# Performance work log

Measured on AMD Instinct MI355X. Metric: run time of the kernel, lower is better.

The kernel has to match this reference:

```python
import jax, jax.numpy as jnp
import numpy as np

B, T, I, H, L, O = 8192, 204, 5, 24, 10, 612

def setup_inputs() -> dict:
    key = jax.random.key(0)
    ks = jax.random.split(key, 10)
    s_ih = 1.0 / np.sqrt(H)
    inp = {
        "x": jax.random.normal(ks[0], (B, T, I), dtype=jnp.float32),
        # torch nn.LSTM params: weight_ih_l0 [4H,I], weight_hh_l0 [4H,H], biases [4H]
        "W_ih": jax.random.uniform(ks[1], (4 * H, I), jnp.float32, -s_ih, s_ih),
        "W_hh": jax.random.uniform(ks[2], (4 * H, H), jnp.float32, -s_ih, s_ih),
        "b_ih": jax.random.uniform(ks[3], (4 * H,), jnp.float32, -s_ih, s_ih),
        "b_hh": jax.random.uniform(ks[4], (4 * H,), jnp.float32, -s_ih, s_ih),
        "fc0_w": jax.random.uniform(ks[5], (L, H * T), jnp.float32, -1 / np.sqrt(H * T), 1 / np.sqrt(H * T)),
        "fc0_b": jax.random.uniform(ks[6], (L,), jnp.float32, -1 / np.sqrt(H * T), 1 / np.sqrt(H * T)),
        "out_w": jax.random.uniform(ks[7], (O, L), jnp.float32, -1 / np.sqrt(L), 1 / np.sqrt(L)),
        "out_b": jax.random.uniform(ks[8], (O,), jnp.float32, -1 / np.sqrt(L), 1 / np.sqrt(L)),
    }
    return inp

def _lstm_forward(x, W_ih, W_hh, b_ih, b_hh):
    # Precompute input projections for all timesteps: [B,T,4H] -> time-major [T,B,4H]
    x_proj = jnp.einsum("bti,gi->btg", x, W_ih) + b_ih
    x_proj = jnp.swapaxes(x_proj, 0, 1)
    h0 = jnp.zeros((x.shape[0], W_hh.shape[1]), x.dtype)
    c0 = jnp.zeros_like(h0)

    def step(carry, xt):
        h, c = carry
        gates = xt + h @ W_hh.T + b_hh  # [B,4H]; torch gate order i,f,g,o
        i, f, g, o = jnp.split(gates, 4, axis=-1)
        c = jax.nn.sigmoid(f) * c + jax.nn.sigmoid(i) * jnp.tanh(g)
        h = jax.nn.sigmoid(o) * jnp.tanh(c)
        return (h, c), h

    _, hs = jax.lax.scan(step, (h0, c0), x_proj)  # hs: [T,B,H]
    return jnp.swapaxes(hs, 0, 1)  # [B,T,H]

def reference(x, W_ih, W_hh, b_ih, b_hh, fc0_w, fc0_b, out_w, out_b):
    h = _lstm_forward(x, W_ih, W_hh, b_ih, b_hh)       # [B,T,H]
    h = h.reshape(h.shape[0], -1)                       # [B, T*H]
    h = jax.nn.relu(h @ fc0_w.T + fc0_b)                # [B, L]
    return h @ out_w.T + out_b                          # [B, O]
```

## Files before the change

kernel.cpp:

```cpp
#include <hip/hip_runtime.h>
#include <math.h>

#define T_  204
#define I_  5
#define H_  24
#define L_  10
#define O_  612
#define Bsz 8192

typedef _Float16 half8 __attribute__((ext_vector_type(8)));
typedef _Float16 half2t __attribute__((ext_vector_type(2)));
typedef float    float4t __attribute__((ext_vector_type(4)));

union U16B { float4t f4; half8 h8; float f[4]; _Float16 h[8]; half2t h2[4]; };

__device__ __forceinline__ float fast_rcp(float x){ return __builtin_amdgcn_rcpf(x); }
__device__ __forceinline__ float fast_ex2(float x){ return __builtin_amdgcn_exp2f(x); }
__device__ __forceinline__ half2t pk2(float a, float b){
    return __builtin_bit_cast(half2t, __builtin_amdgcn_cvt_pkrtz(a, b));
}

#define MFMA16(a,b,c) __builtin_amdgcn_mfma_f32_16x16x32_f16((a),(b),(c),0,0,0)

#define L2E  1.44269504f
#define L2E2 2.88539008f

__device__ __forceinline__ float sigm2(float x){ return fast_rcp(1.f + fast_ex2(x * -L2E)); }
__device__ __forceinline__ float tanh2(float x){ return 2.f * fast_rcp(1.f + fast_ex2(x * -L2E2)) - 1.f; }

__device__ __forceinline__ int unit_of(int q, int T) {
    return (q < 3) ? (8*q + T) : (8*(T >> 1) + 6 + (T & 1));
}

__global__ __launch_bounds__(64)
void pack_fc0(const float* __restrict__ fc0_w, float4t* __restrict__ dst)
{
    const int t = blockIdx.x, lane = threadIdx.x;
    const int m = lane & 15, q = lane >> 4;
    U16B v;
    #pragma unroll
    for (int i = 0; i < 8; ++i) {
        const int k = 8*q + i;
        float f = (m < L_ && k < H_) ? fc0_w[m*(T_*H_) + t*H_ + k] : 0.0f;
        v.h[i] = (_Float16)f;
    }
    dst[t*64 + lane] = v.f4;
}

__global__ __launch_bounds__(64)
void lstm_mfma(const float* __restrict__ x,
               const float* __restrict__ W_ih,
               const float* __restrict__ W_hh,
               const float* __restrict__ b_ih,
               const float* __restrict__ b_hh,
               const float* __restrict__ fc0_b,
               const float* __restrict__ out_w,
               const float* __restrict__ out_b,
               const float4t* __restrict__ fc0A,
               float* __restrict__ out)
{
    __shared__ __align__(16) _Float16 actL[16*24];

    const int lane = threadIdx.x;
    const int m = lane & 15;
    const int q = lane >> 4;
    const int elem = blockIdx.x * 16 + m;

    const float4t zf4 = {0.f, 0.f, 0.f, 0.f};

    half8 Ag[6];
    #pragma unroll
    for (int T6 = 0; T6 < 6; ++T6) {
        const int u = unit_of(m >> 2, T6);
        const int srow = (m & 3) * H_ + u;
        float wv[8];
        if (q < 3) {
            const float4t* pw = (const float4t*)(W_hh + srow*H_ + 8*q);
            float4t wa = pw[0], wb = pw[1];
            #pragma unroll
            for (int i = 0; i < 4; ++i) { wv[i] = wa[i]; wv[4+i] = wb[i]; }
        } else {
            #pragma unroll
            for (int i = 0; i < 8; ++i) wv[i] = 0.f;
            #pragma unroll
            for (int i = 0; i < I_; ++i) wv[i] = W_ih[srow*I_ + i];
            wv[5] = b_ih[srow] + b_hh[srow];
        }
        U16B tw;
        #pragma unroll
        for (int i = 0; i < 8; ++i) tw.h[i] = (_Float16)wv[i];
        Ag[T6] = tw.h8;
    }

    const float* xp = x + (size_t)elem * (T_*I_);

    U16B B;
    if (q == 3) {
        B.h2[0] = pk2(xp[0], xp[1]);
        B.h2[1] = pk2(xp[2], xp[3]);
        B.h2[2] = pk2(xp[4], 1.0f);
        B.h2[3] = pk2(0.f, 0.f);
    } else {
        B.f4 = zf4;
    }
    float xC[I_] = {0,0,0,0,0};
    if (q == 3) {
        #pragma unroll
        for (int i = 0; i < I_; ++i) xC[i] = xp[I_ + i];
    }

    float c_[6] = {0,0,0,0,0,0};
    float4t accF = zf4;
    float4t fa = fc0A[lane];

    for (int t = 0; t < T_; ++t) {
        const int tn = (t + 1 < T_) ? t + 1 : t;
        const float4t fan = fc0A[tn*64 + lane];
        float xN[I_] = {0,0,0,0,0};
        if (q == 3) {
            const int tp2 = (t + 2 < T_) ? t + 2 : T_ - 1;
            const float* xq = xp + tp2*I_;
            #pragma unroll
            for (int i = 0; i < I_; ++i) xN[i] = xq[i];
        }

        float4t D0 = MFMA16(Ag[0], B.h8, zf4);
        float4t D1 = MFMA16(Ag[1], B.h8, zf4);
        float4t D2 = MFMA16(Ag[2], B.h8, zf4);
        float4t D3 = MFMA16(Ag[3], B.h8, zf4);
        float4t D4 = MFMA16(Ag[4], B.h8, zf4);
        float4t D5 = MFMA16(Ag[5], B.h8, zf4);

        float hh[6];
        {
            float4t D[6] = {D0, D1, D2, D3, D4, D5};
            #pragma unroll
            for (int T6 = 0; T6 < 6; ++T6) {
                const float si = sigm2(D[T6][0]);
                const float sf = sigm2(D[T6][1]);
                const float tg = tanh2(D[T6][2]);
                const float so = sigm2(D[T6][3]);
                c_[T6] = fmaf(sf, c_[T6], si * tg);
                hh[T6] = so * tanh2(c_[T6]);
            }
        }

        const float P0 = __builtin_bit_cast(float, pk2(hh[0], hh[1]));
        const float P1 = __builtin_bit_cast(float, pk2(hh[2], hh[3]));
        const float P2 = __builtin_bit_cast(float, pk2(hh[4], hh[5]));

        const int src = 48 + m;
        const float r0 = __shfl(P0, src, 64);
        const float r1 = __shfl(P1, src, 64);
        const float r2 = __shfl(P2, src, 64);
        const float rcv = (q == 0) ? r0 : ((q == 1) ? r1 : r2);

        if (q < 3) {
            B.h2[0] = __builtin_bit_cast(half2t, P0);
            B.h2[1] = __builtin_bit_cast(half2t, P1);
            B.h2[2] = __builtin_bit_cast(half2t, P2);
            B.h2[3] = __builtin_bit_cast(half2t, rcv);
        } else {
            B.h2[0] = pk2(xC[0], xC[1]);
            B.h2[1] = pk2(xC[2], xC[3]);
            B.h2[2] = pk2(xC[4], 1.0f);
            B.h2[3] = pk2(0.f, 0.f);
        }

        U16B fF; fF.f4 = fa;
        accF = MFMA16(fF.h8, B.h8, accF);

        fa = fan;
        #pragma unroll
        for (int i = 0; i < I_; ++i) xC[i] = xN[i];
    }

    float av[4];
    #pragma unroll
    for (int r = 0; r < 4; ++r) {
        const int l = 4*q + r;
        const float fb = (l < L_) ? fc0_b[l] : 0.f;
        const float v = accF[r] + fb;
        av[r] = (l < L_) ? fmaxf(v, 0.f) : 0.f;
    }
    *(half2t*)(&actL[m*24 + 4*q])     = pk2(av[0], av[1]);
    *(half2t*)(&actL[m*24 + 4*q + 2]) = pk2(av[2], av[3]);
    __builtin_amdgcn_wave_barrier();

    U16B Ba;
    if (q < 2) Ba.f4 = *(const float4t*)(&actL[m*24 + q*8]);
    else       Ba.f4 = zf4;

    for (int Tt = 0; Tt < 39; ++Tt) {
        const int row = 16*Tt + m;
        float w0=0.f,w1=0.f,w2=0.f,w3=0.f,w4=0.f,w5=0.f,w6=0.f,w7=0.f;
        if (row < O_ && q < 2) {
            const float2* p2 = (const float2*)(out_w + row*L_);
            if (q == 0) {
                float2 a = p2[0], b = p2[1], cc = p2[2], dd = p2[3];
                w0=a.x; w1=a.y; w2=b.x; w3=b.y; w4=cc.x; w5=cc.y; w6=dd.x; w7=dd.y;
            } else {
                float2 a = p2[4];
                w0=a.x; w1=a.y;
            }
        }
        U16B Aw;
        Aw.h2[0] = pk2(w0,w1); Aw.h2[1] = pk2(w2,w3);
        Aw.h2[2] = pk2(w4,w5); Aw.h2[3] = pk2(w6,w7);

        float4t dd = MFMA16(Aw.h8, Ba.h8, zf4);

        const int ob = 16*Tt + 4*q;
        if (ob < O_) {
            const float4t bias = *(const float4t*)(out_b + ob);
            #pragma unroll
            for (int r = 0; r < 4; ++r) dd[r] += bias[r];
            *(float4t*)(out + (size_t)elem*O_ + ob) = dd;
        }
    }
}

extern "C" void kernel_launch(void* const* d_in, const int* in_sizes, int n_in,
                              void* d_out, int out_size, void* d_ws, size_t ws_size,
                              hipStream_t stream)
{
    const float* x     = (const float*)d_in[0];
    const float* W_ih  = (const float*)d_in[1];
    const float* W_hh  = (const float*)d_in[2];
    const float* b_ih  = (const float*)d_in[3];
    const float* b_hh  = (const float*)d_in[4];
    const float* fc0_w = (const float*)d_in[5];
    const float* fc0_b = (const float*)d_in[6];
    const float* out_w = (const float*)d_in[7];
    const float* out_b = (const float*)d_in[8];
    float* out = (float*)d_out;
    (void)ws_size;

    pack_fc0<<<dim3(T_), dim3(64), 0, stream>>>(fc0_w, (float4t*)d_ws);
    lstm_mfma<<<dim3(Bsz/16), dim3(64), 0, stream>>>(
        x, W_ih, W_hh, b_ih, b_hh, fc0_b, out_w, out_b,
        (const float4t*)d_ws, out);
}
```

Before: 221.9 us.

## Process two batch tiles per wave to interleave independent LSTM recurrences

Each wave now handles 32 batch elements as two independent 16-element tiles, interleaving their MFMAs, gate activations and shuffles to expose instruction-level parallelism in the serial time recurrence. The time loop is unrolled by two with alternating prefetch buffers for x and fc0 weights. The grid is halved, so latency hiding shifts from multiple waves per CU to ILP within one wave, at the cost of higher register use and fewer waves.

After: 357.4 us. 61.1% more time.

```diff
diff --git a/kernel.cpp b/kernel.cpp
--- a/kernel.cpp
+++ b/kernel.cpp
@@ -47,7 +47,89 @@
     dst[t*64 + lane] = v.f4;
 }
 
-__global__ __launch_bounds__(64)
+#define BCH(x) __builtin_bit_cast(half2t, (x))
+
+#define LSTM_STEP(tcur, xCA, xCB, facur)                                        \
+  {                                                                             \
+    float4t DA0 = MFMA16(Ag[0], BA.h8, zf4);                                    \
+    float4t DB0 = MFMA16(Ag[0], BB.h8, zf4);                                    \
+    float4t DA1 = MFMA16(Ag[1], BA.h8, zf4);                                    \
+    float4t DB1 = MFMA16(Ag[1], BB.h8, zf4);                                    \
+    float4t DA2 = MFMA16(Ag[2], BA.h8, zf4);                                    \
+    float4t DB2 = MFMA16(Ag[2], BB.h8, zf4);                                    \
+    float4t DA3 = MFMA16(Ag[3], BA.h8, zf4);                                    \
+    float4t DB3 = MFMA16(Ag[3], BB.h8, zf4);                                    \
+    float4t DA4 = MFMA16(Ag[4], BA.h8, zf4);                                    \
+    float4t DB4 = MFMA16(Ag[4], BB.h8, zf4);                                    \
+    float4t DA5 = MFMA16(Ag[5], BA.h8, zf4);                                    \
+    float4t DB5 = MFMA16(Ag[5], BB.h8, zf4);                                    \
+    float4t DAv[6] = {DA0, DA1, DA2, DA3, DA4, DA5};                            \
+    float4t DBv[6] = {DB0, DB1, DB2, DB3, DB4, DB5};                            \
+    float hA[6];                                                                \
+    float hB[6];                                                                \
+    _Pragma("unroll")                                                           \
+    for (int T6 = 0; T6 < 6; ++T6) {                                            \
+      const float siA = sigm2(DAv[T6][0]);                                      \
+      const float siB = sigm2(DBv[T6][0]);                                      \
+      const float sfA = sigm2(DAv[T6][1]);                                      \
+      const float sfB = sigm2(DBv[T6][1]);                                      \
+      const float tgA = tanh2(DAv[T6][2]);                                      \
+      const float tgB = tanh2(DBv[T6][2]);                                      \
+      const float soA = sigm2(DAv[T6][3]);                                      \
+      const float soB = sigm2(DBv[T6][3]);                                      \
+      cA[T6] = fmaf(sfA, cA[T6], siA * tgA);                                    \
+      cB[T6] = fmaf(sfB, cB[T6], siB * tgB);                                    \
+      hA[T6] = soA * tanh2(cA[T6]);                                             \
+      hB[T6] = soB * tanh2(cB[T6]);                                             \
+    }                                                                           \
+    const float PA0 = __builtin_bit_cast(float, pk2(hA[0], hA[1]));             \
+    const float PA1 = __builtin_bit_cast(float, pk2(hA[2], hA[3]));             \
+    const float PA2 = __builtin_bit_cast(float, pk2(hA[4], hA[5]));             \
+    const float PB0 = __builtin_bit_cast(float, pk2(hB[0], hB[1]));             \
+    const float PB1 = __builtin_bit_cast(float, pk2(hB[2], hB[3]));             \
+    const float PB2 = __builtin_bit_cast(float, pk2(hB[4], hB[5]));             \
+    const int srcl = 48 + m;                                                    \
+    const float rA0 = __shfl(PA0, srcl, 64);                                    \
+    const float rA1 = __shfl(PA1, srcl, 64);                                    \
+    const float rA2 = __shfl(PA2, srcl, 64);                                    \
+    const float rB0 = __shfl(PB0, srcl, 64);                                    \
+    const float rB1 = __shfl(PB1, srcl, 64);                                    \
+    const float rB2 = __shfl(PB2, srcl, 64);                                    \
+    const float rcvA = (q == 0) ? rA0 : ((q == 1) ? rA1 : rA2);                 \
+    const float rcvB = (q == 0) ? rB0 : ((q == 1) ? rB1 : rB2);                 \
+    if (q < 3) {                                                                \
+      BA.h2[0] = BCH(PA0); BA.h2[1] = BCH(PA1);                                 \
+      BA.h2[2] = BCH(PA2); BA.h2[3] = BCH(rcvA);                                \
+      BB.h2[0] = BCH(PB0); BB.h2[1] = BCH(PB1);                                 \
+      BB.h2[2] = BCH(PB2); BB.h2[3] = BCH(rcvB);                                \
+    } else {                                                                    \
+      BA.h2[0] = pk2(xCA[0], xCA[1]);                                           \
+      BA.h2[1] = pk2(xCA[2], xCA[3]);                                           \
+      BA.h2[2] = pk2(xCA[4], 1.0f);                                             \
+      BA.h2[3] = pk2(0.f, 0.f);                                                 \
+      BB.h2[0] = pk2(xCB[0], xCB[1]);                                           \
+      BB.h2[1] = pk2(xCB[2], xCB[3]);                                           \
+      BB.h2[2] = pk2(xCB[4], 1.0f);                                             \
+      BB.h2[3] = pk2(0.f, 0.f);                                                 \
+    }                                                                           \
+    U16B fF; fF.f4 = facur;                                                     \
+    accFA = MFMA16(fF.h8, BA.h8, accFA);                                        \
+    accFB = MFMA16(fF.h8, BB.h8, accFB);                                        \
+    {                                                                           \
+      const int tpx = ((tcur) + 3 < T_) ? (tcur) + 3 : (T_ - 1);                \
+      if (q == 3) {                                                             \
+        _Pragma("unroll")                                                       \
+        for (int i = 0; i < I_; ++i) {                                          \
+          xCA[i] = xpA[tpx * I_ + i];                                           \
+          xCB[i] = xpB[tpx * I_ + i];                                           \
+        }                                                                       \
+      }                                                                         \
+      const int tfx = ((tcur) + 2 < T_) ? (tcur) + 2 : (T_ - 1);                \
+      facur = fc0A[tfx * 64 + lane];                                            \
+    }                                                                           \
+  }
+
+__global__ __launch_bounds__(64, 1)
 void lstm_mfma(const float* __restrict__ x,
                const float* __restrict__ W_ih,
                const float* __restrict__ W_hh,
@@ -59,12 +141,13 @@
                const float4t* __restrict__ fc0A,
                float* __restrict__ out)
 {
-    __shared__ __align__(16) _Float16 actL[16*24];
+    __shared__ __align__(16) _Float16 actL[32*24];
 
     const int lane = threadIdx.x;
     const int m = lane & 15;
     const int q = lane >> 4;
-    const int elem = blockIdx.x * 16 + m;
+    const int elemA = blockIdx.x * 32 + m;
+    const int elemB = elemA + 16;
 
     const float4t zf4 = {0.f, 0.f, 0.f, 0.f};
 
@@ -92,104 +175,71 @@
         Ag[T6] = tw.h8;
     }
 
-    const float* xp = x + (size_t)elem * (T_*I_);
-
-    U16B B;
+    const float* xpA = x + (size_t)elemA * (T_*I_);
+    const float* xpB = x + (size_t)elemB * (T_*I_);
+
+    U16B BA, BB;
     if (q == 3) {
-        B.h2[0] = pk2(xp[0], xp[1]);
-        B.h2[1] = pk2(xp[2], xp[3]);
-        B.h2[2] = pk2(xp[4], 1.0f);
-        B.h2[3] = pk2(0.f, 0.f);
+        BA.h2[0] = pk2(xpA[0], xpA[1]);
+        BA.h2[1] = pk2(xpA[2], xpA[3]);
+        BA.h2[2] = pk2(xpA[4], 1.0f);
+        BA.h2[3] = pk2(0.f, 0.f);
+        BB.h2[0] = pk2(xpB[0], xpB[1]);
+        BB.h2[1] = pk2(xpB[2], xpB[3]);
+        BB.h2[2] = pk2(xpB[4], 1.0f);
+        BB.h2[3] = pk2(0.f, 0.f);
     } else {
-        B.f4 = zf4;
-    }
-    float xC[I_] = {0,0,0,0,0};
+        BA.f4 = zf4;
+        BB.f4 = zf4;
+    }
+
+    float xEA[I_] = {0,0,0,0,0}, xOA[I_] = {0,0,0,0,0};
+    float xEB[I_] = {0,0,0,0,0}, xOB[I_] = {0,0,0,0,0};
     if (q == 3) {
         #pragma unroll
-        for (int i = 0; i < I_; ++i) xC[i] = xp[I_ + i];
-    }
-
-    float c_[6] = {0,0,0,0,0,0};
-    float4t accF = zf4;
-    float4t fa = fc0A[lane];
-
-    for (int t = 0; t < T_; ++t) {
-        const int tn = (t + 1 < T_) ? t + 1 : t;
-        const float4t fan = fc0A[tn*64 + lane];
-        float xN[I_] = {0,0,0,0,0};
-        if (q == 3) {
-            const int tp2 = (t + 2 < T_) ? t + 2 : T_ - 1;
-            const float* xq = xp + tp2*I_;
-            #pragma unroll
-            for (int i = 0; i < I_; ++i) xN[i] = xq[i];
-        }
-
-        float4t D0 = MFMA16(Ag[0], B.h8, zf4);
-        float4t D1 = MFMA16(Ag[1], B.h8, zf4);
-        float4t D2 = MFMA16(Ag[2], B.h8, zf4);
-        float4t D3 = MFMA16(Ag[3], B.h8, zf4);
-        float4t D4 = MFMA16(Ag[4], B.h8, zf4);
-        float4t D5 = MFMA16(Ag[5], B.h8, zf4);
-
-        float hh[6];
-        {
-            float4t D[6] = {D0, D1, D2, D3, D4, D5};
-            #pragma unroll
-            for (int T6 = 0; T6 < 6; ++T6) {
-                const float si = sigm2(D[T6][0]);
-                const float sf = sigm2(D[T6][1]);
-                const float tg = tanh2(D[T6][2]);
-                const float so = sigm2(D[T6][3]);
-                c_[T6] = fmaf(sf, c_[T6], si * tg);
-                hh[T6] = so * tanh2(c_[T6]);
-            }
-        }
-
-        const float P0 = __builtin_bit_cast(float, pk2(hh[0], hh[1]));
-        const float P1 = __builtin_bit_cast(float, pk2(hh[2], hh[3]));
-        const float P2 = __builtin_bit_cast(float, pk2(hh[4], hh[5]));
-
-        const int src = 48 + m;
-        const float r0 = __shfl(P0, src, 64);
-        const float r1 = __shfl(P1, src, 64);
-        const float r2 = __shfl(P2, src, 64);
-        const float rcv = (q == 0) ? r0 : ((q == 1) ? r1 : r2);
-
-        if (q < 3) {
-            B.h2[0] = __builtin_bit_cast(half2t, P0);
-            B.h2[1] = __builtin_bit_cast(half2t, P1);
-            B.h2[2] = __builtin_bit_cast(half2t, P2);
-            B.h2[3] = __builtin_bit_cast(half2t, rcv);
-        } else {
-            B.h2[0] = pk2(xC[0], xC[1]);
-            B.h2[1] = pk2(xC[2], xC[3]);
-            B.h2[2] = pk2(xC[4], 1.0f);
-            B.h2[3] = pk2(0.f, 0.f);
-        }
-
-        U16B fF; fF.f4 = fa;
-        accF = MFMA16(fF.h8, B.h8, accF);
-
-        fa = fan;
-        #pragma unroll
-        for (int i = 0; i < I_; ++i) xC[i] = xN[i];
-    }
-
-    float av[4];
+        for (int i = 0; i < I_; ++i) {
+            xEA[i] = xpA[1*I_ + i];
+            xOA[i] = xpA[2*I_ + i];
+            xEB[i] = xpB[1*I_ + i];
+            xOB[i] = xpB[2*I_ + i];
+        }
+    }
+
+    float cA[6] = {0,0,0,0,0,0};
+    float cB[6] = {0,0,0,0,0,0};
+    float4t accFA = zf4, accFB = zf4;
+    float4t fa0 = fc0A[lane];
+    float4t fa1 = fc0A[64 + lane];
+
+    for (int t = 0; t < T_; t += 2) {
+        LSTM_STEP(t,     xEA, xEB, fa0)
+        LSTM_STEP(t + 1, xOA, xOB, fa1)
+    }
+
+    float avA[4], avB[4];
     #pragma unroll
     for (int r = 0; r < 4; ++r) {
         const int l = 4*q + r;
         const float fb = (l < L_) ? fc0_b[l] : 0.f;
-        const float v = accF[r] + fb;
-        av[r] = (l < L_) ? fmaxf(v, 0.f) : 0.f;
-    }
-    *(half2t*)(&actL[m*24 + 4*q])     = pk2(av[0], av[1]);
-    *(half2t*)(&actL[m*24 + 4*q + 2]) = pk2(av[2], av[3]);
+        const float vA = accFA[r] + fb;
+        const float vB = accFB[r] + fb;
+        avA[r] = (l < L_) ? fmaxf(vA, 0.f) : 0.f;
+        avB[r] = (l < L_) ? fmaxf(vB, 0.f) : 0.f;
+    }
+    *(half2t*)(&actL[m*24 + 4*q])          = pk2(avA[0], avA[1]);
+    *(half2t*)(&actL[m*24 + 4*q + 2])      = pk2(avA[2], avA[3]);
+    *(half2t*)(&actL[(16+m)*24 + 4*q])     = pk2(avB[0], avB[1]);
+    *(half2t*)(&actL[(16+m)*24 + 4*q + 2]) = pk2(avB[2], avB[3]);
     __builtin_amdgcn_wave_barrier();
 
-    U16B Ba;
-    if (q < 2) Ba.f4 = *(const float4t*)(&actL[m*24 + q*8]);
-    else       Ba.f4 = zf4;
+    U16B BaA, BaB;
+    if (q < 2) {
+        BaA.f4 = *(const float4t*)(&actL[m*24 + q*8]);
+        BaB.f4 = *(const float4t*)(&actL[(16+m)*24 + q*8]);
+    } else {
+        BaA.f4 = zf4;
+        BaB.f4 = zf4;
+    }
 
     for (int Tt = 0; Tt < 39; ++Tt) {
         const int row = 16*Tt + m;
@@ -208,14 +258,16 @@
         Aw.h2[0] = pk2(w0,w1); Aw.h2[1] = pk2(w2,w3);
         Aw.h2[2] = pk2(w4,w5); Aw.h2[3] = pk2(w6,w7);
 
-        float4t dd = MFMA16(Aw.h8, Ba.h8, zf4);
+        float4t dA = MFMA16(Aw.h8, BaA.h8, zf4);
+        float4t dB = MFMA16(Aw.h8, BaB.h8, zf4);
 
         const int ob = 16*Tt + 4*q;
         if (ob < O_) {
             const float4t bias = *(const float4t*)(out_b + ob);
             #pragma unroll
-            for (int r = 0; r < 4; ++r) dd[r] += bias[r];
-            *(float4t*)(out + (size_t)elem*O_ + ob) = dd;
+            for (int r = 0; r < 4; ++r) { dA[r] += bias[r]; dB[r] += bias[r]; }
+            *(float4t*)(out + (size_t)elemA*O_ + ob) = dA;
+            *(float4t*)(out + (size_t)elemB*O_ + ob) = dB;
         }
     }
 }
@@ -237,7 +289,7 @@
     (void)ws_size;
 
     pack_fc0<<<dim3(T_), dim3(64), 0, stream>>>(fc0_w, (float4t*)d_ws);
-    lstm_mfma<<<dim3(Bsz/16), dim3(64), 0, stream>>>(
+    lstm_mfma<<<dim3(Bsz/32), dim3(64), 0, stream>>>(
         x, W_ih, W_hh, b_ih, b_hh, fc0_b, out_w, out_b,
         (const float4t*)d_ws, out);
 }
```

## Split LSTM gate tiles across two waves with LDS double-buffered hidden exchange

Applied to the files above, without the earlier changes.

Each 16-element batch tile is now handled by two waves instead of one. Each wave computes three of the six gate MFMA tiles and their activations, and the hidden state is exchanged through a double-buffered LDS buffer with a workgroup barrier every timestep, replacing the cross-lane shuffles. The aim is to halve the serial per-step activation and MFMA work on the recurrence critical path. In exchange it adds an s_barrier and LDS round trip on every step, and the number of resident waves doubles.

After: 218.8 us. No clear change (-1.4%).

```diff
diff --git a/kernel.cpp b/kernel.cpp
--- a/kernel.cpp
+++ b/kernel.cpp
@@ -47,7 +47,54 @@
     dst[t*64 + lane] = v.f4;
 }
 
-__global__ __launch_bounds__(64)
+#define LSTM_STEP(tcur, xC, facur)                                              \
+  {                                                                             \
+    float4t D0 = MFMA16(Ag[0], B.h8, zf4);                                      \
+    float4t D1 = MFMA16(Ag[1], B.h8, zf4);                                      \
+    float4t D2 = MFMA16(Ag[2], B.h8, zf4);                                      \
+    float hh0, hh1, hh2;                                                        \
+    {                                                                           \
+      const float si0 = sigm2(D0[0]), sf0 = sigm2(D0[1]);                       \
+      const float tg0 = tanh2(D0[2]), so0 = sigm2(D0[3]);                       \
+      cc0 = fmaf(sf0, cc0, si0 * tg0);  hh0 = so0 * tanh2(cc0);                 \
+      const float si1 = sigm2(D1[0]), sf1 = sigm2(D1[1]);                       \
+      const float tg1 = tanh2(D1[2]), so1 = sigm2(D1[3]);                       \
+      cc1 = fmaf(sf1, cc1, si1 * tg1);  hh1 = so1 * tanh2(cc1);                 \
+      const float si2 = sigm2(D2[0]), sf2 = sigm2(D2[1]);                       \
+      const float tg2 = tanh2(D2[2]), so2 = sigm2(D2[3]);                       \
+      cc2 = fmaf(sf2, cc2, si2 * tg2);  hh2 = so2 * tanh2(cc2);                 \
+    }                                                                           \
+    const int bofs = ((tcur) & 1) * 384;                                        \
+    const half2t pr = (wv == 0) ? pk2(hh0, hh1) : pk2(hh1, hh2);                \
+    const float  sg = (wv == 0) ? hh2 : hh0;                                    \
+    const half2t sgp = pk2(sg, sg);                                             \
+    *(half2t*)(&hbuf[bofs + pairElem]) = pr;                                    \
+    hbuf[bofs + snglElem] = sgp[0];                                             \
+    asm volatile("s_waitcnt lgkmcnt(0)" ::: "memory");                          \
+    __builtin_amdgcn_s_barrier();                                               \
+    asm volatile("" ::: "memory");                                              \
+    if (q < 3) {                                                                \
+      B.f4 = *(const float4t*)(&hbuf[bofs + m*24 + 8*q]);                       \
+    } else {                                                                    \
+      B.h2[0] = pk2(xC[0], xC[1]);                                              \
+      B.h2[1] = pk2(xC[2], xC[3]);                                              \
+      B.h2[2] = pk2(xC[4], 1.0f);                                               \
+      B.h2[3] = pk2(0.f, 0.f);                                                  \
+    }                                                                           \
+    if (wv == 1) {                                                              \
+      U16B fF; fF.f4 = facur;                                                   \
+      accF = MFMA16(fF.h8, B.h8, accF);                                         \
+      const int tfx = ((tcur) + 2 < T_) ? (tcur) + 2 : (T_ - 1);                \
+      facur = fc0A[tfx * 64 + lane64];                                          \
+    }                                                                           \
+    if (q == 3) {                                                               \
+      const int tpx = ((tcur) + 3 < T_) ? (tcur) + 3 : (T_ - 1);                \
+      _Pragma("unroll")                                                         \
+      for (int i = 0; i < I_; ++i) xC[i] = xp[tpx * I_ + i];                    \
+    }                                                                           \
+  }
+
+__global__ __launch_bounds__(128)
 void lstm_mfma(const float* __restrict__ x,
                const float* __restrict__ W_ih,
                const float* __restrict__ W_hh,
@@ -59,38 +106,48 @@
                const float4t* __restrict__ fc0A,
                float* __restrict__ out)
 {
-    __shared__ __align__(16) _Float16 actL[16*24];
-
-    const int lane = threadIdx.x;
-    const int m = lane & 15;
-    const int q = lane >> 4;
+    __shared__ __align__(16) _Float16 hbuf[2*16*24];
+
+    const int tid  = threadIdx.x;
+    const int lane64 = tid & 63;
+    const int m = tid & 15;
+    const int q = (tid >> 4) & 3;
+    const int wv = tid >> 6;
     const int elem = blockIdx.x * 16 + m;
 
     const float4t zf4 = {0.f, 0.f, 0.f, 0.f};
 
-    half8 Ag[6];
+    half8 Ag[3];
     #pragma unroll
-    for (int T6 = 0; T6 < 6; ++T6) {
-        const int u = unit_of(m >> 2, T6);
+    for (int Tl = 0; Tl < 3; ++Tl) {
+        const int T = 3*wv + Tl;
+        const int u = unit_of(m >> 2, T);
         const int srow = (m & 3) * H_ + u;
-        float wv[8];
+        float wval[8];
         if (q < 3) {
             const float4t* pw = (const float4t*)(W_hh + srow*H_ + 8*q);
             float4t wa = pw[0], wb = pw[1];
             #pragma unroll
-            for (int i = 0; i < 4; ++i) { wv[i] = wa[i]; wv[4+i] = wb[i]; }
+            for (int i = 0; i < 4; ++i) { wval[i] = wa[i]; wval[4+i] = wb[i]; }
         } else {
             #pragma unroll
-            for (int i = 0; i < 8; ++i) wv[i] = 0.f;
-            #pragma unroll
-            for (int i = 0; i < I_; ++i) wv[i] = W_ih[srow*I_ + i];
-            wv[5] = b_ih[srow] + b_hh[srow];
+            for (int i = 0; i < 8; ++i) wval[i] = 0.f;
+            #pragma unroll
+            for (int i = 0; i < I_; ++i) wval[i] = W_ih[srow*I_ + i];
+            wval[5] = b_ih[srow] + b_hh[srow];
         }
         U16B tw;
         #pragma unroll
-        for (int i = 0; i < 8; ++i) tw.h[i] = (_Float16)wv[i];
-        Ag[T6] = tw.h8;
-    }
+        for (int i = 0; i < 8; ++i) tw.h[i] = (_Float16)wval[i];
+        Ag[Tl] = tw.h8;
+    }
+
+    const int u_pair = (wv == 0) ? ((q < 3) ? 8*q     : 6 )
+                                 : ((q < 3) ? 8*q + 4 : 22);
+    const int u_sngl = (wv == 0) ? ((q < 3) ? 8*q + 2 : 14)
+                                 : ((q < 3) ? 8*q + 3 : 15);
+    const int pairElem = m*24 + u_pair;
+    const int snglElem = m*24 + u_sngl;
 
     const float* xp = x + (size_t)elem * (T_*I_);
 
@@ -103,95 +160,51 @@
     } else {
         B.f4 = zf4;
     }
-    float xC[I_] = {0,0,0,0,0};
+
+    float xE[I_] = {0,0,0,0,0}, xO[I_] = {0,0,0,0,0};
     if (q == 3) {
         #pragma unroll
-        for (int i = 0; i < I_; ++i) xC[i] = xp[I_ + i];
-    }
-
-    float c_[6] = {0,0,0,0,0,0};
+        for (int i = 0; i < I_; ++i) {
+            xE[i] = xp[1*I_ + i];
+            xO[i] = xp[2*I_ + i];
+        }
+    }
+
+    float cc0 = 0.f, cc1 = 0.f, cc2 = 0.f;
     float4t accF = zf4;
-    float4t fa = fc0A[lane];
-
-    for (int t = 0; t < T_; ++t) {
-        const int tn = (t + 1 < T_) ? t + 1 : t;
-        const float4t fan = fc0A[tn*64 + lane];
-        float xN[I_] = {0,0,0,0,0};
-        if (q == 3) {
-            const int tp2 = (t + 2 < T_) ? t + 2 : T_ - 1;
-            const float* xq = xp + tp2*I_;
-            #pragma unroll
-            for (int i = 0; i < I_; ++i) xN[i] = xq[i];
-        }
-
-        float4t D0 = MFMA16(Ag[0], B.h8, zf4);
-        float4t D1 = MFMA16(Ag[1], B.h8, zf4);
-        float4t D2 = MFMA16(Ag[2], B.h8, zf4);
-        float4t D3 = MFMA16(Ag[3], B.h8, zf4);
-        float4t D4 = MFMA16(Ag[4], B.h8, zf4);
-        float4t D5 = MFMA16(Ag[5], B.h8, zf4);
-
-        float hh[6];
-        {
-            float4t D[6] = {D0, D1, D2, D3, D4, D5};
-            #pragma unroll
-            for (int T6 = 0; T6 < 6; ++T6) {
-                const float si = sigm2(D[T6][0]);
-                const float sf = sigm2(D[T6][1]);
-                const float tg = tanh2(D[T6][2]);
-                const float so = sigm2(D[T6][3]);
-                c_[T6] = fmaf(sf, c_[T6], si * tg);
-                hh[T6] = so * tanh2(c_[T6]);
-            }
-        }
-
-        const float P0 = __builtin_bit_cast(float, pk2(hh[0], hh[1]));
-        const float P1 = __builtin_bit_cast(float, pk2(hh[2], hh[3]));
-        const float P2 = __builtin_bit_cast(float, pk2(hh[4], hh[5]));
-
-        const int src = 48 + m;
-        const float r0 = __shfl(P0, src, 64);
-        const float r1 = __shfl(P1, src, 64);
-        const float r2 = __shfl(P2, src, 64);
-        const float rcv = (q == 0) ? r0 : ((q == 1) ? r1 : r2);
-
-        if (q < 3) {
-            B.h2[0] = __builtin_bit_cast(half2t, P0);
-            B.h2[1] = __builtin_bit_cast(half2t, P1);
-            B.h2[2] = __builtin_bit_cast(half2t, P2);
-            B.h2[3] = __builtin_bit_cast(half2t, rcv);
-        } else {
-            B.h2[0] = pk2(xC[0], xC[1]);
-            B.h2[1] = pk2(xC[2], xC[3]);
-            B.h2[2] = pk2(xC[4], 1.0f);
-            B.h2[3] = pk2(0.f, 0.f);
-        }
-
-        U16B fF; fF.f4 = fa;
-        accF = MFMA16(fF.h8, B.h8, accF);
-
-        fa = fan;
+    float4t fa0 = zf4, fa1 = zf4;
+    if (wv == 1) {
+        fa0 = fc0A[lane64];
+        fa1 = fc0A[64 + lane64];
+    }
+
+    #pragma unroll 1
+    for (int t = 0; t < T_; t += 2) {
+        LSTM_STEP(t,     xE, fa0)
+        LSTM_STEP(t + 1, xO, fa1)
+    }
+
+    if (wv == 1) {
+        float av[4];
         #pragma unroll
-        for (int i = 0; i < I_; ++i) xC[i] = xN[i];
-    }
-
-    float av[4];
-    #pragma unroll
-    for (int r = 0; r < 4; ++r) {
-        const int l = 4*q + r;
-        const float fb = (l < L_) ? fc0_b[l] : 0.f;
-        const float v = accF[r] + fb;
-        av[r] = (l < L_) ? fmaxf(v, 0.f) : 0.f;
-    }
-    *(half2t*)(&actL[m*24 + 4*q])     = pk2(av[0], av[1]);
-    *(half2t*)(&actL[m*24 + 4*q + 2]) = pk2(av[2], av[3]);
-    __builtin_amdgcn_wave_barrier();
+        for (int r = 0; r < 4; ++r) {
+            const int l = 4*q + r;
+            const float fb = (l < L_) ? fc0_b[l] : 0.f;
+            const float v = accF[r] + fb;
+            av[r] = (l < L_) ? fmaxf(v, 0.f) : 0.f;
+        }
+        *(half2t*)(&hbuf[m*24 + 4*q])     = pk2(av[0], av[1]);
+        *(half2t*)(&hbuf[m*24 + 4*q + 2]) = pk2(av[2], av[3]);
+    }
+    asm volatile("s_waitcnt lgkmcnt(0)" ::: "memory");
+    __builtin_amdgcn_s_barrier();
+    asm volatile("" ::: "memory");
 
     U16B Ba;
-    if (q < 2) Ba.f4 = *(const float4t*)(&actL[m*24 + q*8]);
+    if (q < 2) Ba.f4 = *(const float4t*)(&hbuf[m*24 + q*8]);
     else       Ba.f4 = zf4;
 
-    for (int Tt = 0; Tt < 39; ++Tt) {
+    for (int Tt = wv; Tt < 39; Tt += 2) {
         const int row = 16*Tt + m;
         float w0=0.f,w1=0.f,w2=0.f,w3=0.f,w4=0.f,w5=0.f,w6=0.f,w7=0.f;
         if (row < O_ && q < 2) {
@@ -237,7 +250,7 @@
     (void)ws_size;
 
     pack_fc0<<<dim3(T_), dim3(64), 0, stream>>>(fc0_w, (float4t*)d_ws);
-    lstm_mfma<<<dim3(Bsz/16), dim3(64), 0, stream>>>(
+    lstm_mfma<<<dim3(Bsz/16), dim3(128), 0, stream>>>(
         x, W_ih, W_hh, b_ih, b_hh, fc0_b, out_w, out_b,
         (const float4t*)d_ws, out);
 }
```

## Remap LSTM units to lanes so each lane feeds its own h back

Applied to the files above, without the earlier changes.

The gate-weight matrix is re-laid out so that lane group q (for q<3) owns hidden units 8q..8q+7. Each lane's eight computed h values then land directly in its own MFMA B operand, which removes the three per-step cross-lane shuffles and the select on the serial recurrence path. The cost is eight MFMAs per step instead of six, and activation work on 8 units per lane, with the q==3 lanes taking a divergent branch. The time loop is also manually unrolled by two, with separate prefetch buffers for x and fc0 to hide load latency.

Result: slower. 269.9 us (+21.6%).

```diff
diff --git a/kernel.cpp b/kernel.cpp
--- a/kernel.cpp
+++ b/kernel.cpp
@@ -27,10 +27,6 @@
 
 __device__ __forceinline__ float sigm2(float x){ return fast_rcp(1.f + fast_ex2(x * -L2E)); }
 __device__ __forceinline__ float tanh2(float x){ return 2.f * fast_rcp(1.f + fast_ex2(x * -L2E2)) - 1.f; }
-
-__device__ __forceinline__ int unit_of(int q, int T) {
-    return (q < 3) ? (8*q + T) : (8*(T >> 1) + 6 + (T & 1));
-}
 
 __global__ __launch_bounds__(64)
 void pack_fc0(const float* __restrict__ fc0_w, float4t* __restrict__ dst)
@@ -46,6 +42,51 @@
     }
     dst[t*64 + lane] = v.f4;
 }
+
+#define LSTM_STEP(tcur, xC, facur)                                              \
+  {                                                                             \
+    float4t D0 = MFMA16(Ag[0], B.h8, zf4);                                      \
+    float4t D1 = MFMA16(Ag[1], B.h8, zf4);                                      \
+    float4t D2 = MFMA16(Ag[2], B.h8, zf4);                                      \
+    float4t D3 = MFMA16(Ag[3], B.h8, zf4);                                      \
+    float4t D4 = MFMA16(Ag[4], B.h8, zf4);                                      \
+    float4t D5 = MFMA16(Ag[5], B.h8, zf4);                                      \
+    float4t D6 = MFMA16(Ag[6], B.h8, zf4);                                      \
+    float4t D7 = MFMA16(Ag[7], B.h8, zf4);                                      \
+    if (q < 3) {                                                                \
+      float4t D[8] = {D0, D1, D2, D3, D4, D5, D6, D7};                          \
+      float hh[8];                                                              \
+      _Pragma("unroll")                                                         \
+      for (int T8 = 0; T8 < 8; ++T8) {                                          \
+        const float si = sigm2(D[T8][0]);                                       \
+        const float sf = sigm2(D[T8][1]);                                       \
+        const float tg = tanh2(D[T8][2]);                                       \
+        const float so = sigm2(D[T8][3]);                                       \
+        c_[T8] = fmaf(sf, c_[T8], si * tg);                                     \
+        hh[T8] = so * tanh2(c_[T8]);                                            \
+      }                                                                         \
+      B.h2[0] = pk2(hh[0], hh[1]);                                              \
+      B.h2[1] = pk2(hh[2], hh[3]);                                              \
+      B.h2[2] = pk2(hh[4], hh[5]);                                              \
+      B.h2[3] = pk2(hh[6], hh[7]);                                              \
+    } else {                                                                    \
+      B.h2[0] = pk2(xC[0], xC[1]);                                              \
+      B.h2[1] = pk2(xC[2], xC[3]);                                              \
+      B.h2[2] = pk2(xC[4], 1.0f);                                               \
+      B.h2[3] = pk2(0.f, 0.f);                                                  \
+    }                                                                           \
+    U16B fF; fF.f4 = facur;                                                     \
+    accF = MFMA16(fF.h8, B.h8, accF);                                           \
+    {                                                                           \
+      if (q == 3) {                                                             \
+        const int tpx = ((tcur) + 3 < T_) ? (tcur) + 3 : (T_ - 1);              \
+        _Pragma("unroll")                                                       \
+        for (int i = 0; i < I_; ++i) xC[i] = xp[tpx * I_ + i];                   \
+      }                                                                         \
+      const int tfx = ((tcur) + 2 < T_) ? (tcur) + 2 : (T_ - 1);                \
+      facur = fc0A[tfx * 64 + lane];                                            \
+    }                                                                           \
+  }
 
 __global__ __launch_bounds__(64)
 void lstm_mfma(const float* __restrict__ x,
@@ -68,28 +109,32 @@
 
     const float4t zf4 = {0.f, 0.f, 0.f, 0.f};
 
-    half8 Ag[6];
+    half8 Ag[8];
     #pragma unroll
-    for (int T6 = 0; T6 < 6; ++T6) {
-        const int u = unit_of(m >> 2, T6);
-        const int srow = (m & 3) * H_ + u;
-        float wv[8];
-        if (q < 3) {
-            const float4t* pw = (const float4t*)(W_hh + srow*H_ + 8*q);
-            float4t wa = pw[0], wb = pw[1];
+    for (int T8 = 0; T8 < 8; ++T8) {
+        U16B tw;
+        if (m < 12) {
+            const int u = 8*(m >> 2) + T8;
+            const int srow = (m & 3) * H_ + u;
+            float wv[8];
+            if (q < 3) {
+                const float4t* pw = (const float4t*)(W_hh + srow*H_ + 8*q);
+                float4t wa = pw[0], wb = pw[1];
+                #pragma unroll
+                for (int i = 0; i < 4; ++i) { wv[i] = wa[i]; wv[4+i] = wb[i]; }
+            } else {
+                #pragma unroll
+                for (int i = 0; i < 8; ++i) wv[i] = 0.f;
+                #pragma unroll
+                for (int i = 0; i < I_; ++i) wv[i] = W_ih[srow*I_ + i];
+                wv[5] = b_ih[srow] + b_hh[srow];
+            }
             #pragma unroll
-            for (int i = 0; i < 4; ++i) { wv[i] = wa[i]; wv[4+i] = wb[i]; }
+            for (int i = 0; i < 8; ++i) tw.h[i] = (_Float16)wv[i];
         } else {
-            #pragma unroll
-            for (int i = 0; i < 8; ++i) wv[i] = 0.f;
-            #pragma unroll
-            for (int i = 0; i < I_; ++i) wv[i] = W_ih[srow*I_ + i];
-            wv[5] = b_ih[srow] + b_hh[srow];
-        }
-        U16B tw;
-        #pragma unroll
-        for (int i = 0; i < 8; ++i) tw.h[i] = (_Float16)wv[i];
-        Ag[T6] = tw.h8;
+            tw.f4 = zf4;
+        }
+        Ag[T8] = tw.h8;
     }
 
     const float* xp = x + (size_t)elem * (T_*I_);
@@ -103,76 +148,25 @@
     } else {
         B.f4 = zf4;
     }
-    float xC[I_] = {0,0,0,0,0};
+
+    float xE[I_] = {0,0,0,0,0}, xO[I_] = {0,0,0,0,0};
     if (q == 3) {
         #pragma unroll
-        for (int i = 0; i < I_; ++i) xC[i] = xp[I_ + i];
-    }
-
-    float c_[6] = {0,0,0,0,0,0};
+        for (int i = 0; i < I_; ++i) {
+            xE[i] = xp[1*I_ + i];
+            xO[i] = xp[2*I_ + i];
+        }
+    }
+
+    float c_[8] = {0,0,0,0,0,0,0,0};
     float4t accF = zf4;
-    float4t fa = fc0A[lane];
-
-    for (int t = 0; t < T_; ++t) {
-        const int tn = (t + 1 < T_) ? t + 1 : t;
-        const float4t fan = fc0A[tn*64 + lane];
-        float xN[I_] = {0,0,0,0,0};
-        if (q == 3) {
-            const int tp2 = (t + 2 < T_) ? t + 2 : T_ - 1;
-            const float* xq = xp + tp2*I_;
-            #pragma unroll
-            for (int i = 0; i < I_; ++i) xN[i] = xq[i];
-        }
-
-        float4t D0 = MFMA16(Ag[0], B.h8, zf4);
-        float4t D1 = MFMA16(Ag[1], B.h8, zf4);
-        float4t D2 = MFMA16(Ag[2], B.h8, zf4);
-        float4t D3 = MFMA16(Ag[3], B.h8, zf4);
-        float4t D4 = MFMA16(Ag[4], B.h8, zf4);
-        float4t D5 = MFMA16(Ag[5], B.h8, zf4);
-
-        float hh[6];
-        {
-            float4t D[6] = {D0, D1, D2, D3, D4, D5};
-            #pragma unroll
-            for (int T6 = 0; T6 < 6; ++T6) {
-                const float si = sigm2(D[T6][0]);
-                const float sf = sigm2(D[T6][1]);
-                const float tg = tanh2(D[T6][2]);
-                const float so = sigm2(D[T6][3]);
-                c_[T6] = fmaf(sf, c_[T6], si * tg);
-                hh[T6] = so * tanh2(c_[T6]);
-            }
-        }
-
-        const float P0 = __builtin_bit_cast(float, pk2(hh[0], hh[1]));
-        const float P1 = __builtin_bit_cast(float, pk2(hh[2], hh[3]));
-        const float P2 = __builtin_bit_cast(float, pk2(hh[4], hh[5]));
-
-        const int src = 48 + m;
-        const float r0 = __shfl(P0, src, 64);
-        const float r1 = __shfl(P1, src, 64);
-        const float r2 = __shfl(P2, src, 64);
-        const float rcv = (q == 0) ? r0 : ((q == 1) ? r1 : r2);
-
-        if (q < 3) {
-            B.h2[0] = __builtin_bit_cast(half2t, P0);
-            B.h2[1] = __builtin_bit_cast(half2t, P1);
-            B.h2[2] = __builtin_bit_cast(half2t, P2);
-            B.h2[3] = __builtin_bit_cast(half2t, rcv);
-        } else {
-            B.h2[0] = pk2(xC[0], xC[1]);
-            B.h2[1] = pk2(xC[2], xC[3]);
-            B.h2[2] = pk2(xC[4], 1.0f);
-            B.h2[3] = pk2(0.f, 0.f);
-        }
-
-        U16B fF; fF.f4 = fa;
-        accF = MFMA16(fF.h8, B.h8, accF);
-
-        fa = fan;
-        #pragma unroll
-        for (int i = 0; i < I_; ++i) xC[i] = xN[i];
+    float4t fa0 = fc0A[lane];
+    float4t fa1 = fc0A[64 + lane];
+
+    #pragma unroll 1
+    for (int t = 0; t < T_; t += 2) {
+        LSTM_STEP(t,     xE, fa0)
+        LSTM_STEP(t + 1, xO, fa1)
     }
 
     float av[4];
```
